# Kernel optimization log

Hardware: AMD Instinct MI355X
Metric: run time of the kernel (lower is better)

The kernel has to match this reference:

```python
import jax, jax.numpy as jnp
import numpy as np

N_NODES = 50000
N_EDGES = 800000
NUM_FEATURES = 128
HIDDEN = 128
NUM_CLASSES = 10
NUM_GRAPHS = 512
PROCESSING_STEPS = 4


def setup_inputs() -> dict:
    key = jax.random.key(0)
    ks = jax.random.split(key, 20)
    s = 0.05
    inp = {
        'x': jax.random.normal(ks[0], (N_NODES, NUM_FEATURES), jnp.float32),
        'edge_index': jax.random.randint(ks[1], (2, N_EDGES), 0, N_NODES),
        'batch': jnp.sort(jax.random.randint(ks[2], (N_NODES,), 0, NUM_GRAPHS)),
        # GCN layers (weights stored [in, out])
        'W1': jax.random.normal(ks[3], (NUM_FEATURES, HIDDEN), jnp.float32) * s,
        'b1': jnp.zeros((HIDDEN,), jnp.float32),
        'W2': jax.random.normal(ks[4], (HIDDEN, HIDDEN), jnp.float32) * s,
        'b2': jnp.zeros((HIDDEN,), jnp.float32),
        'W3': jax.random.normal(ks[5], (HIDDEN, HIDDEN), jnp.float32) * s,
        'b3': jnp.zeros((HIDDEN,), jnp.float32),
        # Set2Set LSTM cell: input 2*HIDDEN -> hidden HIDDEN, torch gate order i,f,g,o
        'Wih': jax.random.normal(ks[6], (4 * HIDDEN, 2 * HIDDEN), jnp.float32) * s,
        'Whh': jax.random.normal(ks[7], (4 * HIDDEN, HIDDEN), jnp.float32) * s,
        'bih': jnp.zeros((4 * HIDDEN,), jnp.float32),
        'bhh': jnp.zeros((4 * HIDDEN,), jnp.float32),
        # MLP head
        'L1w': jax.random.normal(ks[8], (2 * HIDDEN, HIDDEN), jnp.float32) * s,
        'L1b': jnp.zeros((HIDDEN,), jnp.float32),
        'L2w': jax.random.normal(ks[9], (HIDDEN, HIDDEN // 2), jnp.float32) * s,
        'L2b': jnp.zeros((HIDDEN // 2,), jnp.float32),
        'L3w': jax.random.normal(ks[10], (HIDDEN // 2, NUM_CLASSES), jnp.float32) * s,
        'L3b': jnp.zeros((NUM_CLASSES,), jnp.float32),
    }
    return inp


def _gcn_conv(x, row, col, W, b, n):
    # PyG GCNConv: x @ W, symmetric normalization with self-loops, scatter-add to targets.
    xw = x @ W  # [N, out]
    deg = jax.ops.segment_sum(jnp.ones_like(col, dtype=xw.dtype), col, num_segments=n)
    dis = jnp.where(deg > 0, jax.lax.rsqrt(jnp.maximum(deg, 1.0)), 0.0)
    norm = dis[row] * dis[col]  # [E+N]
    out = jax.ops.segment_sum(norm[:, None] * xw[row], col, num_segments=n)
    return out + b


def _segment_softmax(e, batch, n_seg):
    emax = jax.lax.stop_gradient(jax.ops.segment_max(e, batch, num_segments=n_seg))
    emax = jnp.where(jnp.isfinite(emax), emax, 0.0)
    a = jnp.exp(e - emax[batch])
    asum = jax.ops.segment_sum(a, batch, num_segments=n_seg)
    return a / jnp.where(asum > 0, asum, 1.0)[batch]


def reference(x, edge_index, batch, W1, b1, W2, b2, W3, b3,
              Wih, Whh, bih, bhh, L1w, L1b, L2w, L2b, L3w, L3b):
    n = x.shape[0]
    # add self loops once
    loops = jnp.arange(n, dtype=edge_index.dtype)
    row = jnp.concatenate([edge_index[0], loops])  # sources
    col = jnp.concatenate([edge_index[1], loops])  # targets

    h = jax.nn.relu(_gcn_conv(x, row, col, W1, b1, n))
    h = jax.nn.relu(_gcn_conv(h, row, col, W2, b2, n))
    h = jax.nn.relu(_gcn_conv(h, row, col, W3, b3, n))

    # Set2Set readout (processing_steps=4)
    d = h.shape[1]
    hs = jnp.zeros((NUM_GRAPHS, d), h.dtype)
    cs = jnp.zeros((NUM_GRAPHS, d), h.dtype)
    q_star = jnp.zeros((NUM_GRAPHS, 2 * d), h.dtype)
    for _ in range(PROCESSING_STEPS):
        gates = q_star @ Wih.T + hs @ Whh.T + bih + bhh  # [B, 4d]
        ig, fg, gg, og = jnp.split(gates, 4, axis=-1)
        cs = jax.nn.sigmoid(fg) * cs + jax.nn.sigmoid(ig) * jnp.tanh(gg)
        q = jax.nn.sigmoid(og) * jnp.tanh(cs)
        hs = q
        e = jnp.sum(h * q[batch], axis=-1)  # [N]
        a = _segment_softmax(e, batch, NUM_GRAPHS)
        r = jax.ops.segment_sum(a[:, None] * h, batch, num_segments=NUM_GRAPHS)
        q_star = jnp.concatenate([q, r], axis=-1)

    # MLP head (dropout inactive in eval)
    y = jax.nn.relu(q_star @ L1w + L1b)
    y = jax.nn.relu(y @ L2w + L2b)
    y = y @ L3w + L3b
    return jax.nn.log_softmax(y, axis=-1)
```

## Files before the change

### kernel.cpp

```cpp
#include <hip/hip_runtime.h>

constexpr int NN  = 50000;
constexpr int NE  = 800000;
constexpr int FD  = 128;
constexpr int NG  = 512;
constexpr int CAP = 96;

typedef __attribute__((ext_vector_type(8))) short bf16x8;
typedef __attribute__((ext_vector_type(4))) float f32x4;

__device__ __forceinline__ float bf2f(unsigned short u) {
    unsigned int v = ((unsigned int)u) << 16;
    float f; __builtin_memcpy(&f, &v, 4); return f;
}
__device__ __forceinline__ unsigned short f2bf(float f) {
    unsigned int u; __builtin_memcpy(&u, &f, 4);
    u += 0x7FFFu + ((u >> 16) & 1u);
    return (unsigned short)(u >> 16);
}
__device__ __forceinline__ float2 bfp(unsigned int u) {
    unsigned int lo = u << 16, hi = u & 0xFFFF0000u;
    float2 r; __builtin_memcpy(&r.x, &lo, 4); __builtin_memcpy(&r.y, &hi, 4);
    return r;
}
__device__ __forceinline__ unsigned int packbf(float a, float b) {
    return (unsigned int)f2bf(a) | ((unsigned int)f2bf(b) << 16);
}
__device__ __forceinline__ float sigmoidf(float x) { return 1.0f / (1.0f + __expf(-x)); }
__device__ __forceinline__ float ldw(const void* p, int idx, int flag) {
    return flag ? ((const float*)p)[idx] : bf2f(((const unsigned short*)p)[idx]);
}

__global__ void k_detect(const unsigned int* __restrict__ xw, int* __restrict__ flag,
                         int* __restrict__ counts) {
    int gid = blockIdx.x * 256 + threadIdx.x;
    if (gid < NN) counts[gid] = 0;
    if (blockIdx.x == 0) {
        __shared__ int cnt;
        if (threadIdx.x == 0) cnt = 0;
        __syncthreads();
        int local = 0;
        for (int i = threadIdx.x; i < 2048; i += 256) {
            unsigned int w = xw[i];
            unsigned int h0 = w & 0xFFFFu, h1 = w >> 16;
            if (((h0 >> 7) & 0xFF) >= 0x90) local++;
            if (((h1 >> 7) & 0xFF) >= 0x90) local++;
        }
        atomicAdd(&cnt, local);
        __syncthreads();
        if (threadIdx.x == 0) *flag = (cnt > 256) ? 1 : 0;
    }
}

__global__ void k_cvt_x(const void* __restrict__ src, unsigned short* __restrict__ dst,
                        const int* __restrict__ batch, int* __restrict__ goff,
                        const int* __restrict__ flagp) {
    int i = blockIdx.x * 256 + threadIdx.x;
    if (i < NN * FD) {
        if (*flagp) dst[i] = f2bf(((const float*)src)[i]);
        else        dst[i] = ((const unsigned short*)src)[i];
    }
    if (i < NN) {
        int b = batch[i];
        if (b < 0) b = 0;
        if (b >= NG) b = NG - 1;
        int prev;
        if (i == 0) prev = -1;
        else {
            prev = batch[i - 1];
            if (prev < 0) prev = 0;
            if (prev >= NG) prev = NG - 1;
        }
        for (int g = prev + 1; g <= b; g++) goff[g] = i;
        if (i == NN - 1)
            for (int g = b + 1; g <= NG; g++) goff[g] = NN;
    }
}

struct WDesc {
    const void* src[16];
    unsigned short* dst[16];
    int off[17];
};
__global__ void k_cvt_w(WDesc d, const int* __restrict__ flagp) {
    int gid = blockIdx.x * 256 + threadIdx.x;
    if (gid >= d.off[16]) return;
    int t = 0;
    while (gid >= d.off[t + 1]) t++;
    int i = gid - d.off[t];
    if (*flagp) d.dst[t][i] = f2bf(((const float*)d.src[t])[i]);
    else        d.dst[t][i] = ((const unsigned short*)d.src[t])[i];
}

__global__ void k_wt(const void* __restrict__ Wih, const void* __restrict__ Whh,
                     const void* __restrict__ bih, const void* __restrict__ bhh,
                     unsigned int* __restrict__ WcombT,
                     unsigned int* __restrict__ WrT,
                     float* __restrict__ bsum, const int* __restrict__ flagp) {
    int gid = blockIdx.x * 256 + threadIdx.x;
    int flag = *flagp;
    if (gid < 64 * 512) {
        int k2 = gid >> 9, row = gid & 511;
        float a0 = ldw(Wih, row * 256 + 2 * k2, flag)     + ldw(Whh, row * 128 + 2 * k2, flag);
        float a1 = ldw(Wih, row * 256 + 2 * k2 + 1, flag) + ldw(Whh, row * 128 + 2 * k2 + 1, flag);
        WcombT[gid] = packbf(a0, a1);
    } else if (gid < 2 * 64 * 512) {
        int g2 = gid - 64 * 512;
        int k2 = g2 >> 9, row = g2 & 511;
        WrT[g2] = packbf(ldw(Wih, row * 256 + 128 + 2 * k2, flag),
                         ldw(Wih, row * 256 + 128 + 2 * k2 + 1, flag));
    } else if (gid < 2 * 64 * 512 + 512) {
        int row = gid - 2 * 64 * 512;
        bsum[row] = ldw(bih, row, flag) + ldw(bhh, row, flag);
    }
}

__global__ void k_fill(const int* __restrict__ ei, int* __restrict__ counts,
                       unsigned short* __restrict__ csr_row) {
    int e = blockIdx.x * 256 + threadIdx.x;
    if (e < NE) {
        int r = ei[e], c = ei[NE + e];
        if ((unsigned)r >= (unsigned)NN) r = 0;
        if ((unsigned)c >= (unsigned)NN) c = 0;
        int pos = atomicAdd(&counts[c], 1);
        if (pos < CAP) csr_row[c * CAP + pos] = (unsigned short)r;
    }
}

__global__ __launch_bounds__(256) void k_gemm(const unsigned short* __restrict__ H,
                                              const unsigned short* __restrict__ W,
                                              unsigned short* __restrict__ XW, int M) {
    __shared__ unsigned short WB[128 * 136];
    int t = threadIdx.x;
    unsigned int* WBu = (unsigned int*)WB;
    for (int idx = t; idx < 128 * 64; idx += 256) {
        int n = idx & 127, k2 = idx >> 7;
        unsigned int u0 = W[(2 * k2) * 128 + n];
        unsigned int u1 = W[(2 * k2 + 1) * 128 + n];
        WBu[n * 68 + k2] = u0 | (u1 << 16);
    }
    __syncthreads();
    int wave = t >> 6, lane = t & 63;
    int lm = lane & 15;
    int lq = lane >> 4;
    int row = blockIdx.x * 64 + wave * 16 + lm;
    int rowc = (row < M) ? row : (M - 1);
    const unsigned short* Arow = H + (size_t)rowc * 128;
    f32x4 acc[8];
#pragma unroll
    for (int n = 0; n < 8; n++) acc[n] = (f32x4){0.f, 0.f, 0.f, 0.f};
#pragma unroll
    for (int kk = 0; kk < 4; kk++) {
        bf16x8 afrag = *(const bf16x8*)(Arow + kk * 32 + lq * 8);
        const unsigned short* wbase = WB + kk * 32 + lq * 8;
#pragma unroll
        for (int n = 0; n < 8; n++) {
            bf16x8 bfrag = *(const bf16x8*)(wbase + (n * 16 + lm) * 136);
            acc[n] = __builtin_amdgcn_mfma_f32_16x16x32_bf16(afrag, bfrag, acc[n], 0, 0, 0);
        }
    }
    int rbase = blockIdx.x * 64 + wave * 16 + lq * 4;
#pragma unroll
    for (int r = 0; r < 4; r++) {
        int orow = rbase + r;
        if (orow < M) {
            unsigned short* orow_p = XW + (size_t)orow * 128 + lm;
#pragma unroll
            for (int n = 0; n < 8; n++) orow_p[n * 16] = f2bf(acc[n][r]);
        }
    }
}

__global__ __launch_bounds__(256) void k_aggr(const unsigned short* __restrict__ XW,
                                              const int* __restrict__ counts,
                                              const unsigned short* __restrict__ csr_row,
                                              const unsigned short* __restrict__ bias,
                                              unsigned short* __restrict__ Hout) {
    int node = blockIdx.x * 8 + (threadIdx.x >> 5);
    int sub = threadIdx.x & 31;
    if (node >= NN) return;
    const uint2* XW2 = (const uint2*)XW;
    int cnt = counts[node];
    float dn = rsqrtf((float)(cnt + 1));
    uint2 sv = XW2[node * 32 + sub];
    float2 s0 = bfp(sv.x), s1 = bfp(sv.y);
    float a0 = dn * s0.x, a1 = dn * s0.y, a2 = dn * s1.x, a3 = dn * s1.y;
    int s = node * CAP;
    int e = s + ((cnt < CAP) ? cnt : CAP);
    int j = s;
    for (; j + 8 <= e; j += 8) {
        int r[8]; float d[8]; uint2 v[8];
#pragma unroll
        for (int k = 0; k < 8; k++) {
            r[k] = csr_row[j + k];
            if (r[k] >= NN) r[k] = 0;
        }
#pragma unroll
        for (int k = 0; k < 8; k++) d[k] = rsqrtf((float)(counts[r[k]] + 1));
#pragma unroll
        for (int k = 0; k < 8; k++) v[k] = XW2[r[k] * 32 + sub];
#pragma unroll
        for (int k = 0; k < 8; k++) {
            float2 f0 = bfp(v[k].x), f1 = bfp(v[k].y);
            a0 += d[k] * f0.x; a1 += d[k] * f0.y;
            a2 += d[k] * f1.x; a3 += d[k] * f1.y;
        }
    }
    for (; j < e; j++) {
        int r = csr_row[j];
        if (r >= NN) r = 0;
        float dr = rsqrtf((float)(counts[r] + 1));
        uint2 v = XW2[r * 32 + sub];
        float2 f0 = bfp(v.x), f1 = bfp(v.y);
        a0 += dr * f0.x; a1 += dr * f0.y;
        a2 += dr * f1.x; a3 += dr * f1.y;
    }
    uint2 bv = ((const uint2*)bias)[sub];
    float2 b0 = bfp(bv.x), b1 = bfp(bv.y);
    uint2 o;
    o.x = packbf(fmaxf(dn * a0 + b0.x, 0.0f), fmaxf(dn * a1 + b0.y, 0.0f));
    o.y = packbf(fmaxf(dn * a2 + b1.x, 0.0f), fmaxf(dn * a3 + b1.y, 0.0f));
    ((uint2*)Hout)[node * 32 + sub] = o;
}

__global__ __launch_bounds__(512) void k_s2s(const unsigned short* __restrict__ H,
                                             const int* __restrict__ goff,
                                             const unsigned int* __restrict__ WcombT,
                                             const unsigned int* __restrict__ WrT,
                                             const float* __restrict__ bsum,
                                             const unsigned short* __restrict__ L1w,
                                             const unsigned short* __restrict__ L1b,
                                             const unsigned short* __restrict__ L2w,
                                             const unsigned short* __restrict__ L2b,
                                             const unsigned short* __restrict__ L3w,
                                             const unsigned short* __restrict__ L3b,
                                             void* __restrict__ out,
                                             const int* __restrict__ flagp) {
    int g = blockIdx.x, t = threadIdx.x;
    __shared__ float qsr[256];
    __shared__ float hsv[128], csv[128];
    __shared__ float gates[512];
    __shared__ float wm[8], wl[8];
    __shared__ float wrr[8][128];
    __shared__ float y1[128], y2[64], y3[10], lseS[1];

    if (t < 256) qsr[t] = 0.0f;
    if (t < 128) { hsv[t] = 0.0f; csv[t] = 0.0f; }
    __syncthreads();

    int s = goff[g], e = goff[g + 1];
    if (s < 0) s = 0;
    if (e > NN) e = NN;
    if (e < s) e = s;
    int w = t >> 6, lane = t & 63;
    const unsigned int* Hu = (const unsigned int*)H;

    for (int step = 0; step < 4; step++) {
        {
            float acc = bsum[t];
#pragma unroll 8
            for (int k2 = 0; k2 < 64; k2++) {
                float2 wv = bfp(WcombT[k2 * 512 + t]);
                acc += wv.x * hsv[2 * k2] + wv.y * hsv[2 * k2 + 1];
            }
#pragma unroll 8
            for (int k2 = 0; k2 < 64; k2++) {
                float2 wv = bfp(WrT[k2 * 512 + t]);
                acc += wv.x * qsr[128 + 2 * k2] + wv.y * qsr[128 + 2 * k2 + 1];
            }
            gates[t] = acc;
        }
        __syncthreads();
        if (t < 128) {
            float ig = sigmoidf(gates[t]),       fg = sigmoidf(gates[128 + t]);
            float gg = tanhf(gates[256 + t]),    og = sigmoidf(gates[384 + t]);
            float c = fg * csv[t] + ig * gg;
            float q = og * tanhf(c);
            csv[t] = c;
            hsv[t] = q;
            qsr[t] = q;
        }
        __syncthreads();

        float qx = hsv[2 * lane], qy = hsv[2 * lane + 1];
        float m = -1e30f, l = 0.0f, r0 = 0.0f, r1 = 0.0f;
        for (int i = s + w; i < e; i += 8) {
            float2 f = bfp(Hu[i * 64 + lane]);
            float p = f.x * qx + f.y * qy;
            for (int d = 32; d > 0; d >>= 1) p += __shfl_xor(p, d);
            float mn = fmaxf(m, p);
            float sc = __expf(m - mn);
            float ep = __expf(p - mn);
            l  = l * sc + ep;
            r0 = r0 * sc + ep * f.x;
            r1 = r1 * sc + ep * f.y;
            m = mn;
        }
        if (lane == 0) { wm[w] = m; wl[w] = l; }
        wrr[w][2 * lane]     = r0;
        wrr[w][2 * lane + 1] = r1;
        __syncthreads();
        if (t < 128) {
            float M = fmaxf(fmaxf(fmaxf(wm[0], wm[1]), fmaxf(wm[2], wm[3])),
                            fmaxf(fmaxf(wm[4], wm[5]), fmaxf(wm[6], wm[7])));
            if (!(M > -1e29f)) M = 0.0f;
            float L = 0.0f, R = 0.0f;
#pragma unroll
            for (int k = 0; k < 8; k++) {
                float sc = __expf(wm[k] - M);
                L += wl[k] * sc;
                R += wrr[k][t] * sc;
            }
            if (!(L > 0.0f)) L = 1.0f;
            qsr[128 + t] = R / L;
        }
        __syncthreads();
    }

    if (t < 128) {
        float acc = bf2f(L1b[t]);
        for (int i = 0; i < 256; i++) acc += bf2f(L1w[i * 128 + t]) * qsr[i];
        y1[t] = fmaxf(acc, 0.0f);
    }
    __syncthreads();
    if (t < 64) {
        float a2 = bf2f(L2b[t]);
        for (int i = 0; i < 128; i++) a2 += bf2f(L2w[i * 64 + t]) * y1[i];
        y2[t] = fmaxf(a2, 0.0f);
    }
    __syncthreads();
    if (t < 10) {
        float a3 = bf2f(L3b[t]);
        for (int i = 0; i < 64; i++) a3 += bf2f(L3w[i * 10 + t]) * y2[i];
        y3[t] = a3;
    }
    __syncthreads();
    if (t == 0) {
        float m = y3[0];
        for (int i = 1; i < 10; i++) m = fmaxf(m, y3[i]);
        float s2 = 0.0f;
        for (int i = 0; i < 10; i++) s2 += __expf(y3[i] - m);
        lseS[0] = m + __logf(s2);
    }
    __syncthreads();
    if (t < 10) {
        float v = y3[t] - lseS[0];
        if (!(v == v)) v = -9.0f;
        if (*flagp) ((float*)out)[g * 10 + t] = v;
        else        ((unsigned short*)out)[g * 10 + t] = f2bf(v);
    }
}

extern "C" void kernel_launch(void* const* d_in, const int* in_sizes, int n_in,
                              void* d_out, int out_size, void* d_ws, size_t ws_size,
                              hipStream_t stream) {
    const int* ei  = (const int*)d_in[1];
    const int* bat = (const int*)d_in[2];

    char* base = (char*)d_ws;
    size_t woff = 0;
    auto alloc = [&](size_t bytes) -> void* {
        void* r = base + woff;
        woff = (woff + bytes + 255) & ~(size_t)255;
        return r;
    };
    unsigned short* A = (unsigned short*)alloc((size_t)NN * FD * 2);
    unsigned short* B = (unsigned short*)alloc((size_t)NN * FD * 2);
    unsigned short* csr_row = (unsigned short*)alloc((size_t)NN * CAP * 2);
    int*   counts   = (int*)alloc(NN * 4);
    int*   goff     = (int*)alloc((NG + 1) * 4);
    int*   flag     = (int*)alloc(256);
    unsigned int* WcombT = (unsigned int*)alloc(64 * 512 * 4);
    unsigned int* WrT    = (unsigned int*)alloc(64 * 512 * 4);
    float* bsum          = (float*)alloc(512 * 4);
    auto walloc = [&](int n) { return (unsigned short*)alloc((size_t)n * 2); };
    unsigned short* cW1  = walloc(128 * 128);
    unsigned short* cb1  = walloc(128);
    unsigned short* cW2  = walloc(128 * 128);
    unsigned short* cb2  = walloc(128);
    unsigned short* cW3  = walloc(128 * 128);
    unsigned short* cb3  = walloc(128);
    unsigned short* cL1w = walloc(256 * 128);
    unsigned short* cL1b = walloc(128);
    unsigned short* cL2w = walloc(128 * 64);
    unsigned short* cL2b = walloc(64);
    unsigned short* cL3w = walloc(64 * 10);
    unsigned short* cL3b = walloc(10);
    (void)ws_size; (void)in_sizes; (void)n_in; (void)out_size;

    const int nblkN = (NN + 255) / 256;
    const int nblkE = (NE + 255) / 256;

    k_detect<<<nblkN, 256, 0, stream>>>((const unsigned int*)d_in[0], flag, counts);
    k_cvt_x<<<(NN * FD + 255) / 256, 256, 0, stream>>>(d_in[0], B, bat, goff, flag);
    {
        WDesc d;
        const int idxs[12] = {3,4,5,6,7,8,13,14,15,16,17,18};
        unsigned short* dsts[12] = {cW1,cb1,cW2,cb2,cW3,cb3,
                                    cL1w,cL1b,cL2w,cL2b,cL3w,cL3b};
        const int ns[12] = {128*128,128,128*128,128,128*128,128,
                            256*128,128,128*64,64,64*10,10};
        int acc = 0;
        for (int i = 0; i < 12; i++) {
            d.src[i] = d_in[idxs[i]];
            d.dst[i] = dsts[i];
            d.off[i] = acc;
            acc += ns[i];
        }
        for (int i = 12; i <= 16; i++) d.off[i] = acc;
        k_cvt_w<<<(acc + 255) / 256, 256, 0, stream>>>(d, flag);
    }
    k_wt<<<(2 * 64 * 512 + 512 + 255) / 256, 256, 0, stream>>>(
        d_in[9], d_in[10], d_in[11], d_in[12], WcombT, WrT, bsum, flag);

    k_fill<<<nblkE, 256, 0, stream>>>(ei, counts, csr_row);

    const int gemmBlk = (NN + 63) / 64;
    const int aggrBlk = (NN + 7) / 8;

    k_gemm<<<gemmBlk, 256, 0, stream>>>(B, cW1, A, NN);
    k_aggr<<<aggrBlk, 256, 0, stream>>>(A, counts, csr_row, cb1, B);
    k_gemm<<<gemmBlk, 256, 0, stream>>>(B, cW2, A, NN);
    k_aggr<<<aggrBlk, 256, 0, stream>>>(A, counts, csr_row, cb2, B);
    k_gemm<<<gemmBlk, 256, 0, stream>>>(B, cW3, A, NN);
    k_aggr<<<aggrBlk, 256, 0, stream>>>(A, counts, csr_row, cb3, B);

    k_s2s<<<NG, 512, 0, stream>>>(B, goff, WcombT, WrT, bsum,
                                  cL1w, cL1b, cL2w, cL2b, cL3w, cL3b,
                                  d_out, flag);
}
```

Measured before the change: 360.2 us.

## Restructure Set2Set attention into chunked block-wide softmax with 4-thread node dot products

Replaces the per-warp serial online softmax, which ran a full 64-lane shuffle reduction for every node, with a chunked scheme. Each 128-node chunk computes its dot products with 4 threads per node using vectorized loads and a padded, replicated q in shared memory. The chunk max and sum are then reduced block-wide, and the weighted feature accumulation is unrolled four nodes at a time. This removes the long shuffle dependency chain per node, at the cost of three block barriers per chunk and reading H twice.

Measured after the change: 360.2 us. About the same (-0.0%).

```diff
diff --git a/kernel.cpp b/kernel.cpp
--- a/kernel.cpp
+++ b/kernel.cpp
@@ -240,8 +240,10 @@
     __shared__ float qsr[256];
     __shared__ float hsv[128], csv[128];
     __shared__ float gates[512];
-    __shared__ float wm[8], wl[8];
+    __shared__ float wred[8];
     __shared__ float wrr[8][128];
+    __shared__ float ps[128];
+    __shared__ float qrep[4 * 132];
     __shared__ float y1[128], y2[64], y3[10], lseS[1];
 
     if (t < 256) qsr[t] = 0.0f;
@@ -254,6 +256,10 @@
     if (e < s) e = s;
     int w = t >> 6, lane = t & 63;
     const unsigned int* Hu = (const unsigned int*)H;
+
+    int nq = t >> 2;
+    int fq = (t & 3) * 16;
+    const float* qc = qrep + (t & 3) * 132 + 2 * fq;
 
     for (int step = 0; step < 4; step++) {
         {
@@ -279,38 +285,79 @@
             csv[t] = c;
             hsv[t] = q;
             qsr[t] = q;
-        }
-        __syncthreads();
-
-        float qx = hsv[2 * lane], qy = hsv[2 * lane + 1];
+            qrep[t] = q; qrep[132 + t] = q; qrep[264 + t] = q; qrep[396 + t] = q;
+        }
+        __syncthreads();
+
         float m = -1e30f, l = 0.0f, r0 = 0.0f, r1 = 0.0f;
-        for (int i = s + w; i < e; i += 8) {
-            float2 f = bfp(Hu[i * 64 + lane]);
-            float p = f.x * qx + f.y * qy;
-            for (int d = 32; d > 0; d >>= 1) p += __shfl_xor(p, d);
-            float mn = fmaxf(m, p);
-            float sc = __expf(m - mn);
-            float ep = __expf(p - mn);
-            l  = l * sc + ep;
-            r0 = r0 * sc + ep * f.x;
-            r1 = r1 * sc + ep * f.y;
-            m = mn;
-        }
-        if (lane == 0) { wm[w] = m; wl[w] = l; }
+        for (int cs = s; cs < e; cs += 128) {
+            int ce = cs + 128; if (ce > e) ce = e;
+            int nid = cs + nq;
+            float eacc = 0.0f;
+            if (nid < ce) {
+                const unsigned int* hrow = Hu + (size_t)nid * 64 + fq;
+#pragma unroll
+                for (int u = 0; u < 16; u += 4) {
+                    uint4 hv = *(const uint4*)(hrow + u);
+                    float2 f0 = bfp(hv.x), f1 = bfp(hv.y);
+                    float2 f2 = bfp(hv.z), f3 = bfp(hv.w);
+                    const float* qp = qc + 2 * u;
+                    eacc += f0.x * qp[0] + f0.y * qp[1] + f1.x * qp[2] + f1.y * qp[3]
+                          + f2.x * qp[4] + f2.y * qp[5] + f3.x * qp[6] + f3.y * qp[7];
+                }
+            }
+            eacc += __shfl_xor(eacc, 1);
+            eacc += __shfl_xor(eacc, 2);
+            float esc = (nid < ce) ? eacc : -1e30f;
+            float vmax = esc;
+            for (int d = 4; d < 64; d <<= 1) vmax = fmaxf(vmax, __shfl_xor(vmax, d));
+            if (lane == 0) wred[w] = vmax;
+            __syncthreads();
+            float M = m;
+#pragma unroll
+            for (int k = 0; k < 8; k++) M = fmaxf(M, wred[k]);
+            float p = __expf(esc - M);
+            bool lead = ((t & 3) == 0) && (nid < ce);
+            if (lead) ps[nq] = p;
+            float psum = lead ? p : 0.0f;
+            for (int d = 1; d < 64; d <<= 1) psum += __shfl_xor(psum, d);
+            __syncthreads();
+            if (lane == 0) wred[w] = psum;
+            __syncthreads();
+            float Lc = 0.0f;
+#pragma unroll
+            for (int k = 0; k < 8; k++) Lc += wred[k];
+            float scale = __expf(m - M);
+            l = l * scale + Lc;
+            r0 *= scale; r1 *= scale;
+            m = M;
+            int i = cs + w;
+            for (; i + 24 < ce; i += 32) {
+                float p0 = ps[i - cs],      p1 = ps[i + 8 - cs];
+                float p2 = ps[i + 16 - cs], p3 = ps[i + 24 - cs];
+                unsigned int v0 = Hu[(size_t)i * 64 + lane];
+                unsigned int v1 = Hu[(size_t)(i + 8) * 64 + lane];
+                unsigned int v2 = Hu[(size_t)(i + 16) * 64 + lane];
+                unsigned int v3 = Hu[(size_t)(i + 24) * 64 + lane];
+                float2 f0 = bfp(v0), f1 = bfp(v1), f2 = bfp(v2), f3 = bfp(v3);
+                r0 += p0 * f0.x + p1 * f1.x + p2 * f2.x + p3 * f3.x;
+                r1 += p0 * f0.y + p1 * f1.y + p2 * f2.y + p3 * f3.y;
+            }
+            for (; i < ce; i += 8) {
+                float p0 = ps[i - cs];
+                float2 f = bfp(Hu[(size_t)i * 64 + lane]);
+                r0 += p0 * f.x; r1 += p0 * f.y;
+            }
+            __syncthreads();
+        }
         wrr[w][2 * lane]     = r0;
         wrr[w][2 * lane + 1] = r1;
         __syncthreads();
         if (t < 128) {
-            float M = fmaxf(fmaxf(fmaxf(wm[0], wm[1]), fmaxf(wm[2], wm[3])),
-                            fmaxf(fmaxf(wm[4], wm[5]), fmaxf(wm[6], wm[7])));
-            if (!(M > -1e29f)) M = 0.0f;
-            float L = 0.0f, R = 0.0f;
-#pragma unroll
-            for (int k = 0; k < 8; k++) {
-                float sc = __expf(wm[k] - M);
-                L += wl[k] * sc;
-                R += wrr[k][t] * sc;
-            }
+            float R = 0.0f;
+#pragma unroll
+            for (int k = 0; k < 8; k++) R += wrr[k][t];
+            float L = l;
             if (!(L > 0.0f)) L = 1.0f;
             qsr[128 + t] = R / L;
         }
```
